# Kernel tuning notes

Measured on AMD Instinct MI355X. Metric: run time of the kernel, lower is better.

The kernel has to match this reference:

```python
import jax, jax.numpy as jnp
import numpy as np

# SREChead (single level, width=0.25): stem 1x1 (128->64) + two 3x3 convs (64->64),
# each Conv->BN(eval, folded into scale/shift)->SiLU, then 1x1 reg (4ch) and obj (1ch)
# heads, followed by YOLOX-style grid decode.
B, C_IN, HGT, WID = 64, 128, 80, 80
C_H = 64            # int(256 * 0.25)
STRIDE = 32


def _conv(x, w):
    # NCHW conv, stride 1, SAME padding (pad=(k-1)//2 as in BaseConv)
    return jax.lax.conv_general_dilated(
        x, w, window_strides=(1, 1), padding='SAME',
        dimension_numbers=('NCHW', 'OIHW', 'NCHW'))


def _bn_silu(y, scale, shift):
    # eval-mode BatchNorm folded to per-channel affine, then SiLU
    return jax.nn.silu(y * scale[None, :, None, None] + shift[None, :, None, None])


def setup_inputs() -> dict:
    key = jax.random.key(0)
    ks = jax.random.split(key, 12)

    def w(k, o, i, kh, kw, s=0.05):
        return jax.random.normal(k, (o, i, kh, kw), jnp.float32) * s

    def bn(k, c):
        k1, k2 = jax.random.split(k)
        scale = 1.0 + 0.1 * jax.random.normal(k1, (c,), jnp.float32)
        shift = 0.05 * jax.random.normal(k2, (c,), jnp.float32)
        return scale, shift

    stem_scale, stem_shift = bn(ks[2], C_H)
    c1_scale, c1_shift = bn(ks[4], C_H)
    c2_scale, c2_shift = bn(ks[6], C_H)
    return {
        'x': jax.random.normal(ks[0], (B, C_IN, HGT, WID), jnp.float32),
        'stem_w': w(ks[1], C_H, C_IN, 1, 1),
        'stem_scale': stem_scale, 'stem_shift': stem_shift,
        'c1_w': w(ks[3], C_H, C_H, 3, 3),
        'c1_scale': c1_scale, 'c1_shift': c1_shift,
        'c2_w': w(ks[5], C_H, C_H, 3, 3),
        'c2_scale': c2_scale, 'c2_shift': c2_shift,
        'reg_w': w(ks[7], 4, C_H, 1, 1),
        'reg_b': jnp.zeros((4,), jnp.float32),
        'obj_w': w(ks[8], 1, C_H, 1, 1),
        'obj_b': jnp.zeros((1,), jnp.float32),
    }


def reference(x, stem_w, stem_scale, stem_shift,
              c1_w, c1_scale, c1_shift,
              c2_w, c2_scale, c2_shift,
              reg_w, reg_b, obj_w, obj_b):
    f = _bn_silu(_conv(x, stem_w), stem_scale, stem_shift)       # [B,64,H,W]
    f = _bn_silu(_conv(f, c1_w), c1_scale, c1_shift)
    f = _bn_silu(_conv(f, c2_w), c2_scale, c2_shift)
    reg = _conv(f, reg_w) + reg_b[None, :, None, None]           # [B,4,H,W]
    obj = jax.nn.sigmoid(_conv(f, obj_w) + obj_b[None, :, None, None])  # [B,1,H,W]
    out = jnp.concatenate([reg, obj], axis=1)                    # [B,5,H,W]
    out = out.reshape(out.shape[0], 5, HGT * WID).transpose(0, 2, 1)  # [B,HW,5]
    # YOLOX decode: xy = (pred_xy + grid) * stride, wh = exp(pred_wh) * stride
    yv, xv = jnp.meshgrid(jnp.arange(HGT), jnp.arange(WID), indexing='ij')
    grid = jnp.stack([xv, yv], -1).reshape(1, HGT * WID, 2).astype(out.dtype)
    xy = (out[..., :2] + grid) * STRIDE
    wh = jnp.exp(out[..., 2:4]) * STRIDE
    return jnp.concatenate([xy, wh, out[..., 4:5]], axis=-1)     # [B,HW,5]
```

## Files before the change

### kernel.cpp

```cpp
#include <hip/hip_runtime.h>
#include <cstdint>


typedef short short8 __attribute__((ext_vector_type(8)));
typedef float floatx4 __attribute__((ext_vector_type(4)));
typedef float fx4 __attribute__((ext_vector_type(4)));
typedef unsigned short us4 __attribute__((ext_vector_type(4)));
typedef unsigned uint4v __attribute__((ext_vector_type(4)));
typedef unsigned uint2v __attribute__((ext_vector_type(2)));

#define NPIX 6400
#define CGS  3952
#define CGS2 2576

static __device__ __forceinline__ unsigned short f2bf(float f) {
    unsigned u = __builtin_bit_cast(unsigned, f);
    u += 0x7fffu + ((u >> 16) & 1u);
    return (unsigned short)(u >> 16);
}

static __device__ __forceinline__ unsigned cvt_pk_bf16(float a, float b) {
    unsigned r;
    asm("v_cvt_pk_bf16_f32 %0, %1, %2" : "=v"(r) : "v"(a), "v"(b));
    return r;
}

static __device__ __forceinline__ float silu_(float v) {
    return v / (1.0f + __expf(-v));
}

__global__ __launch_bounds__(256) void rearr_w_kernel(
    const float* __restrict__ ws_, const float* __restrict__ w1,
    const float* __restrict__ w2,
    unsigned short* __restrict__ wS, unsigned short* __restrict__ wB1,
    unsigned short* __restrict__ wB2) {
    int idx = blockIdx.x * 256 + threadIdx.x;
    if (idx < 8192) {
        int e = idx;
        int j = e & 7, lane = (e >> 3) & 63, ct = (e >> 9) & 3, kb = e >> 11;
        int co = ct * 16 + (lane & 15);
        int ci = kb * 32 + ((lane >> 4) * 8) + j;
        wS[e] = f2bf(ws_[co * 128 + ci]);
        return;
    }
    idx -= 8192;
    const float* src = (idx < 36864) ? w1 : w2;
    unsigned short* dst = (idx < 36864) ? wB1 : wB2;
    int e = (idx < 36864) ? idx : idx - 36864;
    int j = e & 7, lane = (e >> 3) & 63, ct = (e >> 9) & 3, kb = e >> 11;
    int co = ct * 16 + (lane & 15);
    int k = kb * 32 + ((lane >> 4) * 8) + j;
    int ci = k & 63, tap = k >> 6;
    dst[e] = f2bf(src[(co * 64 + ci) * 9 + tap]);
}

__global__ __launch_bounds__(256) void stem_kernel(
    const float* __restrict__ x, const unsigned short* __restrict__ wS,
    const float* __restrict__ scale, const float* __restrict__ shift,
    unsigned short* __restrict__ f1) {
    int b = blockIdx.y;
    int tid = threadIdx.x;
    int pbase = blockIdx.x * 128;
    int lane = tid & 63, wv = tid >> 6;
    int l15 = lane & 15, q = lane >> 4;

    floatx4 acc[4][2];
    floatx4 zf = {0.0f, 0.0f, 0.0f, 0.0f};
    #pragma unroll
    for (int ct = 0; ct < 4; ++ct)
        #pragma unroll
        for (int t = 0; t < 2; ++t) acc[ct][t] = zf;

    const float* xb = x + (size_t)b * 128 * NPIX + pbase + wv * 32 + l15;

    #pragma unroll
    for (int kb = 0; kb < 4; ++kb) {
        short8 wf[4];
        #pragma unroll
        for (int ct = 0; ct < 4; ++ct)
            wf[ct] = *(const short8*)(wS + ((kb * 4 + ct) * 64 + lane) * 8);
        short8 xf[2];
        #pragma unroll
        for (int t = 0; t < 2; ++t) {
            const float* src = xb + (size_t)(kb * 32 + q * 8) * NPIX + t * 16;
            float v[8];
            #pragma unroll
            for (int j = 0; j < 8; ++j) v[j] = src[(size_t)j * NPIX];
            uint4v u;
            #pragma unroll
            for (int j = 0; j < 4; ++j) u[j] = cvt_pk_bf16(v[2 * j], v[2 * j + 1]);
            xf[t] = __builtin_bit_cast(short8, u);
        }
        #pragma unroll
        for (int ct = 0; ct < 4; ++ct)
            #pragma unroll
            for (int t = 0; t < 2; ++t)
                acc[ct][t] = __builtin_amdgcn_mfma_f32_16x16x32_bf16(
                    wf[ct], xf[t], acc[ct][t], 0, 0, 0);
    }

    float sc[4][4], sh[4][4];
    #pragma unroll
    for (int ct = 0; ct < 4; ++ct)
        #pragma unroll
        for (int r = 0; r < 4; ++r) {
            sc[ct][r] = scale[ct * 16 + q * 4 + r];
            sh[ct][r] = shift[ct * 16 + q * 4 + r];
        }

    #pragma unroll
    for (int t = 0; t < 2; ++t) {
        int pg = pbase + (wv * 2 + t) * 16 + l15;
        unsigned short* dst = f1 + ((size_t)b * NPIX + pg) * 64;
        #pragma unroll
        for (int ct = 0; ct < 4; ++ct) {
            float r0 = silu_(acc[ct][t][0] * sc[ct][0] + sh[ct][0]);
            float r1 = silu_(acc[ct][t][1] * sc[ct][1] + sh[ct][1]);
            float r2 = silu_(acc[ct][t][2] * sc[ct][2] + sh[ct][2]);
            float r3 = silu_(acc[ct][t][3] * sc[ct][3] + sh[ct][3]);
            uint2v p2 = {cvt_pk_bf16(r0, r1), cvt_pk_bf16(r2, r3)};
            *(us4*)(dst + ct * 16 + q * 4) = __builtin_bit_cast(us4, p2);
        }
    }
}

static __device__ __forceinline__ void conv_core(
    const unsigned short* __restrict__ fin, const unsigned short* __restrict__ wB,
    unsigned short* tile, floatx4 (*acc)[5], int b, int y0,
    int tid, int lane, int wv, int l15, int q) {
    const unsigned short* fb = fin + (size_t)b * NPIX * 64;
    floatx4 zf = {0.0f, 0.0f, 0.0f, 0.0f};
    #pragma unroll
    for (int c4 = 0; c4 < 4; ++c4)
        #pragma unroll
        for (int pt = 0; pt < 5; ++pt) acc[c4][pt] = zf;

    #pragma unroll
    for (int half = 0; half < 2; ++half) {
        if (half) __syncthreads();
        #pragma unroll
        for (int i = 0; i < 8; ++i) {
            int cid = i * 256 + tid;
            if (cid < 1968) {
                int pixL = cid >> 2, g = cid & 3;
                int r = pixL / 82, c = pixL - r * 82;
                int gy = y0 - 1 + r, gx = c - 1;
                short8 v = {};
                if ((unsigned)gy < 80u && (unsigned)gx < 80u)
                    v = *(const short8*)(
                        fb + (size_t)(gy * 80 + gx) * 64 + half * 32 + g * 8);
                *(short8*)(tile + g * CGS + pixL * 8) = v;
            }
        }
        __syncthreads();

        #pragma unroll
        for (int trow = 0; trow < 3; ++trow) {
            const int dy = trow - 1;
            #pragma unroll
            for (int tc = 0; tc < 3; ++tc) {
                const int dx = tc - 1;
                const int kb = (trow * 3 + tc) * 2 + half;
                short8 w4[4];
                #pragma unroll
                for (int c4 = 0; c4 < 4; ++c4)
                    w4[c4] = *(const short8*)(wB + ((kb * 4 + c4) * 64 + lane) * 8);
                #pragma unroll
                for (int pt = 0; pt < 5; ++pt) {
                    int pix = (wv + 1 + dy) * 82 + pt * 16 + l15 + 1 + dx;
                    short8 b8 = *(const short8*)(tile + q * CGS + pix * 8);
                    #pragma unroll
                    for (int c4 = 0; c4 < 4; ++c4)
                        acc[c4][pt] = __builtin_amdgcn_mfma_f32_16x16x32_bf16(
                            w4[c4], b8, acc[c4][pt], 0, 0, 0);
                }
            }
        }
    }
}

__global__ __launch_bounds__(256, 3) void conv3_kernel(
    const unsigned short* __restrict__ fin, const unsigned short* __restrict__ wB,
    const float* __restrict__ scale, const float* __restrict__ shift,
    unsigned short* __restrict__ fout) {
    __shared__ __align__(16) unsigned short tile[8 * CGS2];
    int b = blockIdx.y, y0 = blockIdx.x * 4;
    int tid = threadIdx.x;
    int lane = tid & 63, wv = tid >> 6;
    int l15 = lane & 15, q = lane >> 4;

    floatx4 acc[4][5];
    conv_core(fin, wB, tile, acc, b, y0, tid, lane, wv, l15, q);

    float sc4[4][4], sh4[4][4];
    #pragma unroll
    for (int c4 = 0; c4 < 4; ++c4)
        #pragma unroll
        for (int r = 0; r < 4; ++r) {
            sc4[c4][r] = scale[c4 * 16 + q * 4 + r];
            sh4[c4][r] = shift[c4 * 16 + q * 4 + r];
        }
    #pragma unroll
    for (int pt = 0; pt < 5; ++pt) {
        int pg = (y0 + wv) * 80 + pt * 16 + l15;
        unsigned short* dst = fout + ((size_t)b * NPIX + pg) * 64;
        #pragma unroll
        for (int c4 = 0; c4 < 4; ++c4) {
            float r0 = silu_(acc[c4][pt][0] * sc4[c4][0] + sh4[c4][0]);
            float r1 = silu_(acc[c4][pt][1] * sc4[c4][1] + sh4[c4][1]);
            float r2 = silu_(acc[c4][pt][2] * sc4[c4][2] + sh4[c4][2]);
            float r3 = silu_(acc[c4][pt][3] * sc4[c4][3] + sh4[c4][3]);
            uint2v p2 = {cvt_pk_bf16(r0, r1), cvt_pk_bf16(r2, r3)};
            *(us4*)(dst + c4 * 16 + q * 4) = __builtin_bit_cast(us4, p2);
        }
    }
}

__global__ __launch_bounds__(256, 3) void conv_head_kernel(
    const unsigned short* __restrict__ fin, const unsigned short* __restrict__ wB,
    const float* __restrict__ scale, const float* __restrict__ shift,
    const float* __restrict__ reg_w, const float* __restrict__ reg_b,
    const float* __restrict__ obj_w, const float* __restrict__ obj_b,
    float* __restrict__ out) {
    __shared__ __align__(16) unsigned short tile[8 * CGS2];
    int b = blockIdx.y, y0 = blockIdx.x * 4;
    int tid = threadIdx.x;
    int lane = tid & 63, wv = tid >> 6;
    int l15 = lane & 15, q = lane >> 4;

    floatx4 acc[4][5];
    conv_core(fin, wB, tile, acc, b, y0, tid, lane, wv, l15, q);

    __syncthreads();

    float sc4[4][4], sh4[4][4];
    #pragma unroll
    for (int c4 = 0; c4 < 4; ++c4)
        #pragma unroll
        for (int r = 0; r < 4; ++r) {
            sc4[c4][r] = scale[c4 * 16 + q * 4 + r];
            sh4[c4][r] = shift[c4 * 16 + q * 4 + r];
        }
    #pragma unroll
    for (int pt = 0; pt < 5; ++pt) {
        int pix = wv * 80 + pt * 16 + l15;
        #pragma unroll
        for (int c4 = 0; c4 < 4; ++c4) {
            int gco = c4 * 2 + (q >> 1);
            float r0 = silu_(acc[c4][pt][0] * sc4[c4][0] + sh4[c4][0]);
            float r1 = silu_(acc[c4][pt][1] * sc4[c4][1] + sh4[c4][1]);
            float r2 = silu_(acc[c4][pt][2] * sc4[c4][2] + sh4[c4][2]);
            float r3 = silu_(acc[c4][pt][3] * sc4[c4][3] + sh4[c4][3]);
            uint2v p2 = {cvt_pk_bf16(r0, r1), cvt_pk_bf16(r2, r3)};
            *(us4*)(tile + gco * CGS2 + pix * 8 + (q & 1) * 4) =
                __builtin_bit_cast(us4, p2);
        }
    }

    short8 hbf[2];
    #pragma unroll
    for (int kb2 = 0; kb2 < 2; ++kb2) {
        int k0 = kb2 * 32 + q * 8;
        short8 f = {};
        if (l15 < 4) {
            #pragma unroll
            for (int j = 0; j < 8; ++j) f[j] = (short)f2bf(reg_w[l15 * 64 + k0 + j]);
        } else if (l15 == 4) {
            #pragma unroll
            for (int j = 0; j < 8; ++j) f[j] = (short)f2bf(obj_w[k0 + j]);
        }
        hbf[kb2] = f;
    }

    __syncthreads();

    floatx4 zf = {0.0f, 0.0f, 0.0f, 0.0f};
    floatx4 acc5[5];
    #pragma unroll
    for (int t = 0; t < 5; ++t) acc5[t] = zf;
    #pragma unroll
    for (int t = 0; t < 5; ++t) {
        int mt = wv * 5 + t;
        int pix = mt * 16 + l15;
        #pragma unroll
        for (int kb2 = 0; kb2 < 2; ++kb2) {
            short8 a = *(const short8*)(tile + (kb2 * 4 + q) * CGS2 + pix * 8);
            acc5[t] = __builtin_amdgcn_mfma_f32_16x16x32_bf16(
                a, hbf[kb2], acc5[t], 0, 0, 0);
        }
    }

    float bias = 0.0f;
    if (l15 < 4) bias = reg_b[l15];
    else if (l15 == 4) bias = obj_b[0];

    #pragma unroll
    for (int t = 0; t < 5; ++t) {
        int mt = wv * 5 + t;
        #pragma unroll
        for (int r = 0; r < 4; ++r) {
            int pixL = mt * 16 + q * 4 + r;
            if (l15 < 5) {
                float v = acc5[t][r] + bias;
                float gx = (float)(pixL % 80);
                float gy = (float)(y0 + pixL / 80);
                float o;
                if (l15 == 0)      o = (v + gx) * 32.0f;
                else if (l15 == 1) o = (v + gy) * 32.0f;
                else if (l15 < 4)  o = __expf(v) * 32.0f;
                else               o = 1.0f / (1.0f + __expf(-v));
                out[((size_t)b * NPIX + y0 * 80 + pixL) * 5 + l15] = o;
            }
        }
    }
}

extern "C" void kernel_launch(void* const* d_in, const int* in_sizes, int n_in,
                              void* d_out, int out_size, void* d_ws, size_t ws_size,
                              hipStream_t stream) {
    const float* x          = (const float*)d_in[0];
    const float* stem_w     = (const float*)d_in[1];
    const float* stem_scale = (const float*)d_in[2];
    const float* stem_shift = (const float*)d_in[3];
    const float* c1_w       = (const float*)d_in[4];
    const float* c1_scale   = (const float*)d_in[5];
    const float* c1_shift   = (const float*)d_in[6];
    const float* c2_w       = (const float*)d_in[7];
    const float* c2_scale   = (const float*)d_in[8];
    const float* c2_shift   = (const float*)d_in[9];
    const float* reg_w      = (const float*)d_in[10];
    const float* reg_b      = (const float*)d_in[11];
    const float* obj_w      = (const float*)d_in[12];
    const float* obj_b      = (const float*)d_in[13];
    float* out = (float*)d_out;

    const size_t needed = ((size_t)8192 + 73728 + 2 * (size_t)64 * NPIX * 64) * 2;
    if (ws_size < needed) return;

    unsigned short* ws  = (unsigned short*)d_ws;
    unsigned short* wS  = ws;
    unsigned short* wB1 = ws + 8192;
    unsigned short* wB2 = wB1 + 36864;
    unsigned short* f1  = wB2 + 36864;
    unsigned short* f2  = f1 + (size_t)64 * NPIX * 64;

    rearr_w_kernel<<<320, 256, 0, stream>>>(stem_w, c1_w, c2_w, wS, wB1, wB2);
    stem_kernel<<<dim3(50, 64), 256, 0, stream>>>(x, wS, stem_scale, stem_shift, f1);
    conv3_kernel<<<dim3(20, 64), 256, 0, stream>>>(f1, wB1, c1_scale, c1_shift, f2);
    conv_head_kernel<<<dim3(20, 64), 256, 0, stream>>>(f2, wB2, c2_scale, c2_shift,
                                                       reg_w, reg_b, obj_w, obj_b, out);
}
```

Baseline: 441.7 us.

## Fuse all stages into one persistent cooperative kernel with grid syncs

Replaces four separate kernel launches with one persistent cooperative kernel. Blocks loop over the weight-rearrange, stem, conv1 and head tiles, with grid-wide syncs between stages. The goal is to remove launch gaps and the tail idle time between dependent kernels. In exchange it adds grid barrier costs, fixed-size grid scheduling that can leave tiles unevenly spread (1280 tiles over 768 blocks), and an extra __syncthreads at the start of each conv tile.

```diff
diff --git a/kernel.cpp b/kernel.cpp
--- a/kernel.cpp
+++ b/kernel.cpp
@@ -1,5 +1,8 @@
 #include <hip/hip_runtime.h>
+#include <hip/hip_cooperative_groups.h>
 #include <cstdint>
+
+namespace cg = cooperative_groups;
 
 
 typedef short short8 __attribute__((ext_vector_type(8)));
@@ -29,12 +32,12 @@
     return v / (1.0f + __expf(-v));
 }
 
-__global__ __launch_bounds__(256) void rearr_w_kernel(
-    const float* __restrict__ ws_, const float* __restrict__ w1,
+
+static __device__ __forceinline__ void rearr_elem(
+    int idx, const float* __restrict__ ws_, const float* __restrict__ w1,
     const float* __restrict__ w2,
     unsigned short* __restrict__ wS, unsigned short* __restrict__ wB1,
     unsigned short* __restrict__ wB2) {
-    int idx = blockIdx.x * 256 + threadIdx.x;
     if (idx < 8192) {
         int e = idx;
         int j = e & 7, lane = (e >> 3) & 63, ct = (e >> 9) & 3, kb = e >> 11;
@@ -54,16 +57,11 @@
     dst[e] = f2bf(src[(co * 64 + ci) * 9 + tap]);
 }
 
-__global__ __launch_bounds__(256) void stem_kernel(
+static __device__ __forceinline__ void stem_tile(
     const float* __restrict__ x, const unsigned short* __restrict__ wS,
     const float* __restrict__ scale, const float* __restrict__ shift,
-    unsigned short* __restrict__ f1) {
-    int b = blockIdx.y;
-    int tid = threadIdx.x;
-    int pbase = blockIdx.x * 128;
-    int lane = tid & 63, wv = tid >> 6;
-    int l15 = lane & 15, q = lane >> 4;
-
+    unsigned short* __restrict__ f1, int b, int pbase,
+    int lane, int wv, int l15, int q) {
     floatx4 acc[4][2];
     floatx4 zf = {0.0f, 0.0f, 0.0f, 0.0f};
     #pragma unroll
@@ -137,7 +135,7 @@
 
     #pragma unroll
     for (int half = 0; half < 2; ++half) {
-        if (half) __syncthreads();
+        __syncthreads();
         #pragma unroll
         for (int i = 0; i < 8; ++i) {
             int cid = i * 256 + tid;
@@ -179,16 +177,11 @@
     }
 }
 
-__global__ __launch_bounds__(256, 3) void conv3_kernel(
+static __device__ __forceinline__ void conv3_tile(
     const unsigned short* __restrict__ fin, const unsigned short* __restrict__ wB,
     const float* __restrict__ scale, const float* __restrict__ shift,
-    unsigned short* __restrict__ fout) {
-    __shared__ __align__(16) unsigned short tile[8 * CGS2];
-    int b = blockIdx.y, y0 = blockIdx.x * 4;
-    int tid = threadIdx.x;
-    int lane = tid & 63, wv = tid >> 6;
-    int l15 = lane & 15, q = lane >> 4;
-
+    unsigned short* __restrict__ fout, unsigned short* tile, int b, int y0,
+    int tid, int lane, int wv, int l15, int q) {
     floatx4 acc[4][5];
     conv_core(fin, wB, tile, acc, b, y0, tid, lane, wv, l15, q);
 
@@ -216,18 +209,13 @@
     }
 }
 
-__global__ __launch_bounds__(256, 3) void conv_head_kernel(
+static __device__ __forceinline__ void head_tile(
     const unsigned short* __restrict__ fin, const unsigned short* __restrict__ wB,
     const float* __restrict__ scale, const float* __restrict__ shift,
     const float* __restrict__ reg_w, const float* __restrict__ reg_b,
     const float* __restrict__ obj_w, const float* __restrict__ obj_b,
-    float* __restrict__ out) {
-    __shared__ __align__(16) unsigned short tile[8 * CGS2];
-    int b = blockIdx.y, y0 = blockIdx.x * 4;
-    int tid = threadIdx.x;
-    int lane = tid & 63, wv = tid >> 6;
-    int l15 = lane & 15, q = lane >> 4;
-
+    float* __restrict__ out, unsigned short* tile, int b, int y0,
+    int tid, int lane, int wv, int l15, int q) {
     floatx4 acc[4][5];
     conv_core(fin, wB, tile, acc, b, y0, tid, lane, wv, l15, q);
 
@@ -313,6 +301,96 @@
             }
         }
     }
+}
+
+__global__ __launch_bounds__(256, 3) void mega_kernel(
+    const float* __restrict__ x,
+    const float* __restrict__ stem_w, const float* __restrict__ stem_scale,
+    const float* __restrict__ stem_shift,
+    const float* __restrict__ c1_w, const float* __restrict__ c1_scale,
+    const float* __restrict__ c1_shift,
+    const float* __restrict__ c2_w, const float* __restrict__ c2_scale,
+    const float* __restrict__ c2_shift,
+    const float* __restrict__ reg_w, const float* __restrict__ reg_b,
+    const float* __restrict__ obj_w, const float* __restrict__ obj_b,
+    float* __restrict__ out,
+    unsigned short* __restrict__ wS, unsigned short* __restrict__ wB1,
+    unsigned short* __restrict__ wB2, unsigned short* __restrict__ f1,
+    unsigned short* __restrict__ f2) {
+    __shared__ __align__(16) unsigned short tile[8 * CGS2];
+    int tid = threadIdx.x;
+    int lane = tid & 63, wv = tid >> 6;
+    int l15 = lane & 15, q = lane >> 4;
+    int gsz = gridDim.x;
+
+    for (int idx = blockIdx.x * 256 + tid; idx < 81920; idx += gsz * 256)
+        rearr_elem(idx, stem_w, c1_w, c2_w, wS, wB1, wB2);
+    __threadfence();
+    cg::this_grid().sync();
+
+    for (int t = blockIdx.x; t < 3200; t += gsz) {
+        int b = t / 50, pbase = (t - b * 50) * 128;
+        stem_tile(x, wS, stem_scale, stem_shift, f1, b, pbase, lane, wv, l15, q);
+    }
+    __threadfence();
+    cg::this_grid().sync();
+
+    for (int t = blockIdx.x; t < 1280; t += gsz) {
+        int b = t / 20, y0 = (t - b * 20) * 4;
+        conv3_tile(f1, wB1, c1_scale, c1_shift, f2, tile, b, y0,
+                   tid, lane, wv, l15, q);
+    }
+    __threadfence();
+    cg::this_grid().sync();
+
+    for (int t = blockIdx.x; t < 1280; t += gsz) {
+        int b = t / 20, y0 = (t - b * 20) * 4;
+        head_tile(f2, wB2, c2_scale, c2_shift, reg_w, reg_b, obj_w, obj_b,
+                  out, tile, b, y0, tid, lane, wv, l15, q);
+    }
+}
+
+__global__ __launch_bounds__(256) void rearr_w_kernel(
+    const float* __restrict__ ws_, const float* __restrict__ w1,
+    const float* __restrict__ w2,
+    unsigned short* __restrict__ wS, unsigned short* __restrict__ wB1,
+    unsigned short* __restrict__ wB2) {
+    int idx = blockIdx.x * 256 + threadIdx.x;
+    if (idx < 81920) rearr_elem(idx, ws_, w1, w2, wS, wB1, wB2);
+}
+
+__global__ __launch_bounds__(256) void stem_kernel(
+    const float* __restrict__ x, const unsigned short* __restrict__ wS,
+    const float* __restrict__ scale, const float* __restrict__ shift,
+    unsigned short* __restrict__ f1) {
+    int tid = threadIdx.x;
+    int lane = tid & 63, wv = tid >> 6;
+    stem_tile(x, wS, scale, shift, f1, blockIdx.y, blockIdx.x * 128,
+              lane, wv, lane & 15, lane >> 4);
+}
+
+__global__ __launch_bounds__(256, 3) void conv3_kernel(
+    const unsigned short* __restrict__ fin, const unsigned short* __restrict__ wB,
+    const float* __restrict__ scale, const float* __restrict__ shift,
+    unsigned short* __restrict__ fout) {
+    __shared__ __align__(16) unsigned short tile[8 * CGS2];
+    int tid = threadIdx.x;
+    int lane = tid & 63, wv = tid >> 6;
+    conv3_tile(fin, wB, scale, shift, fout, tile, blockIdx.y, blockIdx.x * 4,
+               tid, lane, wv, lane & 15, lane >> 4);
+}
+
+__global__ __launch_bounds__(256, 3) void conv_head_kernel(
+    const unsigned short* __restrict__ fin, const unsigned short* __restrict__ wB,
+    const float* __restrict__ scale, const float* __restrict__ shift,
+    const float* __restrict__ reg_w, const float* __restrict__ reg_b,
+    const float* __restrict__ obj_w, const float* __restrict__ obj_b,
+    float* __restrict__ out) {
+    __shared__ __align__(16) unsigned short tile[8 * CGS2];
+    int tid = threadIdx.x;
+    int lane = tid & 63, wv = tid >> 6;
+    head_tile(fin, wB, scale, shift, reg_w, reg_b, obj_w, obj_b, out, tile,
+              blockIdx.y, blockIdx.x * 4, tid, lane, wv, lane & 15, lane >> 4);
 }
 
 extern "C" void kernel_launch(void* const* d_in, const int* in_sizes, int n_in,
@@ -344,9 +422,36 @@
     unsigned short* f1  = wB2 + 36864;
     unsigned short* f2  = f1 + (size_t)64 * NPIX * 64;
 
-    rearr_w_kernel<<<320, 256, 0, stream>>>(stem_w, c1_w, c2_w, wS, wB1, wB2);
-    stem_kernel<<<dim3(50, 64), 256, 0, stream>>>(x, wS, stem_scale, stem_shift, f1);
-    conv3_kernel<<<dim3(20, 64), 256, 0, stream>>>(f1, wB1, c1_scale, c1_shift, f2);
-    conv_head_kernel<<<dim3(20, 64), 256, 0, stream>>>(f2, wB2, c2_scale, c2_shift,
-                                                       reg_w, reg_b, obj_w, obj_b, out);
-}
+    static int nblk = 0;
+    if (nblk == 0) {
+        int perCU = 0;
+        if (hipOccupancyMaxActiveBlocksPerMultiprocessor(
+                &perCU, (const void*)mega_kernel, 256, 0) != hipSuccess ||
+            perCU <= 0)
+            perCU = 2;
+        if (perCU > 3) perCU = 3;
+        nblk = perCU * 256;
+    }
+
+    void* args[] = {
+        (void*)&x,
+        (void*)&stem_w, (void*)&stem_scale, (void*)&stem_shift,
+        (void*)&c1_w, (void*)&c1_scale, (void*)&c1_shift,
+        (void*)&c2_w, (void*)&c2_scale, (void*)&c2_shift,
+        (void*)&reg_w, (void*)&reg_b, (void*)&obj_w, (void*)&obj_b,
+        (void*)&out,
+        (void*)&wS, (void*)&wB1, (void*)&wB2, (void*)&f1, (void*)&f2};
+
+    hipError_t e = hipLaunchCooperativeKernel(
+        (const void*)mega_kernel, dim3(nblk), dim3(256), args, 0, stream);
+
+    if (e != hipSuccess) {
+        rearr_w_kernel<<<320, 256, 0, stream>>>(stem_w, c1_w, c2_w, wS, wB1, wB2);
+        stem_kernel<<<dim3(50, 64), 256, 0, stream>>>(x, wS, stem_scale,
+                                                      stem_shift, f1);
+        conv3_kernel<<<dim3(20, 64), 256, 0, stream>>>(f1, wB1, c1_scale,
+                                                       c1_shift, f2);
+        conv_head_kernel<<<dim3(20, 64), 256, 0, stream>>>(
+            f2, wB2, c2_scale, c2_shift, reg_w, reg_b, obj_w, obj_b, out);
+    }
+}
```

Result: slower. 1.083 ms (+145.2%).
